# Kernel optimization log

Measured on AMD Instinct MI355X. Metric: run time of the kernel, lower is better.

The kernel has to match this reference:

```python
import jax, jax.numpy as jnp
import numpy as np

B, S, QS, KS, F, H = 4, 2048, 512, 1024, 1024, 16
DH = F // H  # head dim = 64


def setup_inputs() -> dict:
    key = jax.random.key(0)
    ks = jax.random.split(key, 7)
    s = 0.02
    return {
        "x": jax.random.normal(ks[0], (B, S, QS), dtype=jnp.float32),
        "y": jax.random.normal(ks[1], (B, S, QS), dtype=jnp.float32),
        "z": jax.random.normal(ks[2], (B, S, KS), dtype=jnp.float32),
        "Wq": jax.random.normal(ks[3], (2 * QS, F), dtype=jnp.float32) * s,
        "Wk": jax.random.normal(ks[4], (KS, F), dtype=jnp.float32) * s,
        "Wv": jax.random.normal(ks[5], (KS, F), dtype=jnp.float32) * s,
        "Wo": jax.random.normal(ks[6], (F, F), dtype=jnp.float32) * s,
    }


def _split_heads(t):
    # [B, S, F] -> [B, H, S, DH]
    return t.reshape(B, S, H, DH).transpose(0, 2, 1, 3)


def reference(x, y, z, Wq, Wk, Wv, Wo):
    q = _split_heads(jnp.concatenate([x, y], axis=-1) @ Wq)  # [B,H,S,DH]
    k = _split_heads(z @ Wk)
    v = _split_heads(z @ Wv)
    scale = 1.0 / jnp.sqrt(jnp.asarray(DH, dtype=q.dtype))
    scores = jnp.einsum("bhsd,bhtd->bhst", q, k) * scale  # [B,H,S,S]
    attn = jax.nn.softmax(scores, axis=-1)
    out = jnp.einsum("bhst,bhtd->bhsd", attn, v)  # [B,H,S,DH]
    out = out.transpose(0, 2, 1, 3).reshape(B, S, F)
    return out @ Wo
```

## Files before the change

kernel.cpp:

```cpp
#include <hip/hip_runtime.h>

typedef __attribute__((ext_vector_type(8))) short short8;
typedef __attribute__((ext_vector_type(4))) float f32x4;
typedef __attribute__((ext_vector_type(16))) float f32x16;
typedef __attribute__((ext_vector_type(4))) unsigned short us4;
typedef __attribute__((ext_vector_type(4))) unsigned int u32x4;

#define GLOAD16(gsrc, ldst)                                             \
  __builtin_amdgcn_global_load_lds(                                     \
      (const __attribute__((address_space(1))) unsigned int*)(gsrc),    \
      (__attribute__((address_space(3))) unsigned int*)(ldst), 16, 0, 0)

#define VMEM_DRAIN_BARRIER()                              \
  do {                                                    \
    asm volatile("s_waitcnt vmcnt(0)" ::: "memory");      \
    __builtin_amdgcn_sched_barrier(0);                    \
    __syncthreads();                                      \
  } while (0)

#if __has_builtin(__builtin_amdgcn_exp2f)
#define EXP2F(x) __builtin_amdgcn_exp2f(x)
#else
#define EXP2F(x) exp2f(x)
#endif

static __device__ __forceinline__ unsigned short f2bf(float f) {
  unsigned int u = __float_as_uint(f);
  u += 0x7fffu + ((u >> 16) & 1u);
  return (unsigned short)(u >> 16);
}

static __device__ __forceinline__ unsigned cvtpk(float lo, float hi) {
  unsigned r;
  asm("v_cvt_pk_bf16_f32 %0, %1, %2" : "=v"(r) : "v"(lo), "v"(hi));
  return r;
}

__global__ __launch_bounds__(256) void prep(const float* __restrict__ x,
                                            const float* __restrict__ y,
                                            const float* __restrict__ z,
                                            const float* __restrict__ Wq,
                                            const float* __restrict__ Wk,
                                            const float* __restrict__ Wv,
                                            const float* __restrict__ Wo,
                                            unsigned short* __restrict__ XY,
                                            unsigned short* __restrict__ Z,
                                            unsigned short* __restrict__ WqT,
                                            unsigned short* __restrict__ WkT,
                                            unsigned short* __restrict__ WvT,
                                            unsigned short* __restrict__ WoT) {
  __shared__ __align__(16) unsigned short LT[64 * 72];
  const int bid = blockIdx.x, t = threadIdx.x;

  if (bid < 2048) {
    const int NX = (8192 * 512) / 4;
    const int NZ = (8192 * 1024) / 4;
    const int total = 2 * NX + NZ;
    for (int idx = bid * 256 + t; idx < total; idx += 2048 * 256) {
      const float* src;
      unsigned short* dst;
      if (idx < NX) {
        int p = idx * 4; int row = p >> 9, c = p & 511;
        src = x + p; dst = XY + (size_t)row * 1024 + c;
      } else if (idx < 2 * NX) {
        int p = (idx - NX) * 4; int row = p >> 9, c = p & 511;
        src = y + p; dst = XY + (size_t)row * 1024 + 512 + c;
      } else {
        int p = (idx - 2 * NX) * 4;
        src = z + p; dst = Z + p;
      }
      float4 v = *(const float4*)src;
      us4 o; o[0] = f2bf(v.x); o[1] = f2bf(v.y); o[2] = f2bf(v.z); o[3] = f2bf(v.w);
      *(us4*)dst = o;
    }
    return;
  }

  const int seg = (bid - 2048) >> 8;
  const int local = (bid - 2048) & 255;
  const float* W = (seg == 0) ? Wq : (seg == 1) ? Wk : (seg == 2) ? Wv : Wo;
  unsigned short* WT = (seg == 0) ? WqT : (seg == 1) ? WkT : (seg == 2) ? WvT : WoT;
  const int k0 = (local >> 4) * 64, n0 = (local & 15) * 64;
#pragma unroll
  for (int j = 0; j < 4; ++j) {
    int r = j * 16 + (t >> 4);
    int c = (t & 15) * 4;
    float4 w = *(const float4*)(W + (size_t)(k0 + r) * 1024 + n0 + c);
    LT[(c + 0) * 72 + r] = f2bf(w.x);
    LT[(c + 1) * 72 + r] = f2bf(w.y);
    LT[(c + 2) * 72 + r] = f2bf(w.z);
    LT[(c + 3) * 72 + r] = f2bf(w.w);
  }
  __syncthreads();
#pragma unroll
  for (int j = 0; j < 2; ++j) {
    int n = j * 32 + (t >> 3), ch = t & 7;
    *(short8*)(WT + (size_t)(n0 + n) * 1024 + k0 + ch * 8) =
        *(const short8*)(LT + n * 72 + ch * 8);
  }
}

__global__ __launch_bounds__(256) void qkv_gemm(const unsigned short* __restrict__ XY,
                                                const unsigned short* __restrict__ Zb,
                                                const unsigned short* __restrict__ WqT,
                                                const unsigned short* __restrict__ WkT,
                                                const unsigned short* __restrict__ WvT,
                                                unsigned short* __restrict__ Qb,
                                                unsigned short* __restrict__ Kb,
                                                unsigned short* __restrict__ Vb) {
  __shared__ __align__(16) unsigned short As[2][128 * 32];
  __shared__ __align__(16) unsigned short Bs[2][128 * 32];
  const int tid = threadIdx.x;
  const int lane = tid & 63, wid = tid >> 6;
  const int lq = lane & 15, lg = lane >> 4;
  const int wr = wid >> 1, wc = wid & 1;
  const int seg = blockIdx.x >> 3;
  const int m0 = blockIdx.y * 128, n0 = (blockIdx.x & 7) * 128;

  const unsigned short* A;
  const unsigned short* Bt;
  unsigned short* C;
  float scale;
  if (seg == 0)      { A = XY; Bt = WqT; C = Qb; scale = 0.18033688011112042f; }
  else if (seg == 1) { A = Zb; Bt = WkT; C = Kb; scale = 1.0f; }
  else               { A = Zb; Bt = WvT; C = Vb; scale = 1.0f; }

  const int sr = tid >> 2, sc = tid & 3;

#define GSTAGE(bf, kk)                                                       \
  do {                                                                       \
    _Pragma("unroll")                                                        \
    for (int i = 0; i < 2; ++i) {                                            \
      int r = i * 64 + sr;                                                   \
      int c = sc ^ ((r >> 1) & 3);                                           \
      GLOAD16(A + (size_t)(m0 + r) * 1024 + (kk) + c * 8,                    \
              (char*)As[bf] + wid * 1024 + i * 4096);                        \
      GLOAD16(Bt + (size_t)(n0 + r) * 1024 + (kk) + c * 8,                   \
              (char*)Bs[bf] + wid * 1024 + i * 4096);                        \
    }                                                                        \
  } while (0)

  f32x4 acc[4][4] = {};
  GSTAGE(0, 0);
  VMEM_DRAIN_BARRIER();
  int buf = 0;

  for (int k0 = 0; k0 < 1024; k0 += 32) {
    if (k0 + 32 < 1024) GSTAGE(buf ^ 1, k0 + 32);
    short8 af[4], bfr[4];
#pragma unroll
    for (int mf = 0; mf < 4; ++mf) {
      int r = wr * 64 + mf * 16 + lq;
      int c = lg ^ ((r >> 1) & 3);
      af[mf] = *(const short8*)(As[buf] + r * 32 + c * 8);
    }
#pragma unroll
    for (int nf = 0; nf < 4; ++nf) {
      int r = wc * 64 + nf * 16 + lq;
      int c = lg ^ ((r >> 1) & 3);
      bfr[nf] = *(const short8*)(Bs[buf] + r * 32 + c * 8);
    }
#pragma unroll
    for (int mf = 0; mf < 4; ++mf)
#pragma unroll
      for (int nf = 0; nf < 4; ++nf)
        acc[mf][nf] = __builtin_amdgcn_mfma_f32_16x16x32_bf16(af[mf], bfr[nf],
                                                              acc[mf][nf], 0, 0, 0);
    VMEM_DRAIN_BARRIER();
    buf ^= 1;
  }
#undef GSTAGE

#pragma unroll
  for (int mf = 0; mf < 4; ++mf)
#pragma unroll
    for (int nf = 0; nf < 4; ++nf)
#pragma unroll
      for (int j = 0; j < 4; ++j) {
        int row = m0 + wr * 64 + mf * 16 + lg * 4 + j;
        int col = n0 + wc * 64 + nf * 16 + lq;
        C[(size_t)row * 1024 + col] = f2bf(acc[mf][nf][j] * scale);
      }
}

__global__ __launch_bounds__(256) void gemm_nt(const unsigned short* __restrict__ A,
                                               const unsigned short* __restrict__ Bt,
                                               float* __restrict__ Cout) {
  __shared__ __align__(16) unsigned short As[2][128 * 32];
  __shared__ __align__(16) unsigned short Bs[2][128 * 32];
  const int tid = threadIdx.x;
  const int lane = tid & 63, wid = tid >> 6;
  const int lq = lane & 15, lg = lane >> 4;
  const int wr = wid >> 1, wc = wid & 1;
  const int m0 = blockIdx.y * 128, n0 = blockIdx.x * 128;
  const int sr = tid >> 2, sc = tid & 3;

#define GSTAGE(bf, kk)                                                       \
  do {                                                                       \
    _Pragma("unroll")                                                        \
    for (int i = 0; i < 2; ++i) {                                            \
      int r = i * 64 + sr;                                                   \
      int c = sc ^ ((r >> 1) & 3);                                           \
      GLOAD16(A + (size_t)(m0 + r) * 1024 + (kk) + c * 8,                    \
              (char*)As[bf] + wid * 1024 + i * 4096);                        \
      GLOAD16(Bt + (size_t)(n0 + r) * 1024 + (kk) + c * 8,                   \
              (char*)Bs[bf] + wid * 1024 + i * 4096);                        \
    }                                                                        \
  } while (0)

  f32x4 acc[4][4] = {};
  GSTAGE(0, 0);
  VMEM_DRAIN_BARRIER();
  int buf = 0;

  for (int k0 = 0; k0 < 1024; k0 += 32) {
    if (k0 + 32 < 1024) GSTAGE(buf ^ 1, k0 + 32);
    short8 af[4], bfr[4];
#pragma unroll
    for (int mf = 0; mf < 4; ++mf) {
      int r = wr * 64 + mf * 16 + lq;
      int c = lg ^ ((r >> 1) & 3);
      af[mf] = *(const short8*)(As[buf] + r * 32 + c * 8);
    }
#pragma unroll
    for (int nf = 0; nf < 4; ++nf) {
      int r = wc * 64 + nf * 16 + lq;
      int c = lg ^ ((r >> 1) & 3);
      bfr[nf] = *(const short8*)(Bs[buf] + r * 32 + c * 8);
    }
#pragma unroll
    for (int mf = 0; mf < 4; ++mf)
#pragma unroll
      for (int nf = 0; nf < 4; ++nf)
        acc[mf][nf] = __builtin_amdgcn_mfma_f32_16x16x32_bf16(af[mf], bfr[nf],
                                                              acc[mf][nf], 0, 0, 0);
    VMEM_DRAIN_BARRIER();
    buf ^= 1;
  }
#undef GSTAGE

#pragma unroll
  for (int mf = 0; mf < 4; ++mf)
#pragma unroll
    for (int nf = 0; nf < 4; ++nf)
#pragma unroll
      for (int j = 0; j < 4; ++j) {
        int row = m0 + wr * 64 + mf * 16 + lg * 4 + j;
        int col = n0 + wc * 64 + nf * 16 + lq;
        Cout[(size_t)row * 1024 + col] = acc[mf][nf][j];
      }
}

__global__ __launch_bounds__(256) void vtrans(const unsigned short* __restrict__ V,
                                              unsigned short* __restrict__ Vt) {
  __shared__ __align__(16) unsigned short LT[64 * 72];
  const int bh = blockIdx.y, b = bh >> 4, h = bh & 15;
  const int s0 = blockIdx.x * 64;
  const int t = threadIdx.x;
#pragma unroll
  for (int i = 0; i < 2; ++i) {
    int r = i * 32 + (t >> 3);
    int c = t & 7;
    short8 v = *(const short8*)(V + (size_t)(b * 2048 + s0 + r) * 1024 + h * 64 + c * 8);
#pragma unroll
    for (int e = 0; e < 8; ++e)
      LT[(c * 8 + e) * 72 + r] = (unsigned short)v[e];
  }
  __syncthreads();
#pragma unroll
  for (int i = 0; i < 2; ++i) {
    int d = i * 32 + (t >> 3);
    int c = t & 7;
    *(short8*)(Vt + ((size_t)bh * 64 + d) * 2048 + s0 + c * 8) =
        *(const short8*)(LT + d * 72 + c * 8);
  }
}

__global__ __launch_bounds__(256, 4) void attn7(const unsigned short* __restrict__ Q,
                                                const unsigned short* __restrict__ K,
                                                const unsigned short* __restrict__ Vt,
                                                unsigned short* __restrict__ AO) {
  __shared__ __align__(16) unsigned short Ks[2][64 * 64];
  __shared__ __align__(16) unsigned short Vs[2][64 * 64];

  const int lin = blockIdx.x + (blockIdx.y << 4);
  const int xcd = lin & 7, rest = lin >> 3;
  const int bh = xcd * 8 + (rest >> 4);
  const int q0 = (rest & 15) * 128;
  const int b = bh >> 4, h = bh & 15;

  const int tid = threadIdx.x, lane = tid & 63, w = tid >> 6;
  const int l31 = lane & 31, hi = lane >> 5;
  const int swz = l31 & 7;

  short8 qf[4];
#pragma unroll
  for (int dblk = 0; dblk < 4; ++dblk)
    qf[dblk] = *(const short8*)(Q + (size_t)(b * 2048 + q0 + w * 32 + l31) * 1024 +
                                h * 64 + dblk * 16 + hi * 8);

  short8 ones;
#pragma unroll
  for (int e = 0; e < 8; ++e) ones[e] = (short)0x3F80;

#define STAGE(bf, t)                                                               \
  do {                                                                             \
    _Pragma("unroll")                                                              \
    for (int i = 0; i < 2; ++i) {                                                  \
      int ch = i * 256 + tid;                                                      \
      int r = ch >> 3, c = ch & 7, g = c ^ (r & 7);                                \
      GLOAD16(K + (size_t)(b * 2048 + (t) * 64 + r) * 1024 + h * 64 + g * 8,       \
              (char*)Ks[bf] + i * 4096 + w * 1024);                                \
    }                                                                              \
    _Pragma("unroll")                                                              \
    for (int i = 0; i < 2; ++i) {                                                  \
      int ch = i * 256 + tid;                                                      \
      int r = ch >> 3, c = ch & 7, g = c ^ (r & 7);                                \
      GLOAD16(Vt + ((size_t)bh * 64 + r) * 2048 + (t) * 64 + g * 8,                \
              (char*)Vs[bf] + i * 4096 + w * 1024);                                \
    }                                                                              \
  } while (0)

  STAGE(0, 0);
  VMEM_DRAIN_BARRIER();

  f32x16 od[2] = {};
  f32x16 sums = {};
  int buf = 0;

  for (int t = 0; t < 32; ++t) {
    if (t < 31) STAGE(buf ^ 1, t + 1);

    f32x16 st[2];
    __builtin_amdgcn_s_setprio(1);
#pragma unroll
    for (int kh = 0; kh < 2; ++kh) {
      f32x16 a = {};
#pragma unroll
      for (int dblk = 0; dblk < 4; ++dblk) {
        short8 kf = *(const short8*)(Ks[buf] + (kh * 32 + l31) * 64 +
                                     (((dblk * 2 + hi) ^ swz) * 8));
        a = __builtin_amdgcn_mfma_f32_32x32x16_bf16(kf, qf[dblk], a, 0, 0, 0);
      }
      st[kh] = a;
    }
    __builtin_amdgcn_s_setprio(0);

#pragma unroll
    for (int kh = 0; kh < 2; ++kh)
#pragma unroll
      for (int r = 0; r < 16; ++r) st[kh][r] = EXP2F(st[kh][r]);

    __builtin_amdgcn_s_setprio(1);
#pragma unroll
    for (int ks = 0; ks < 4; ++ks) {
      const int tt = ks >> 1, cm = (ks & 1) * 2;
      unsigned a_lo = cvtpk(st[tt][cm * 4 + 0], st[tt][cm * 4 + 1]);
      unsigned a_hi = cvtpk(st[tt][cm * 4 + 2], st[tt][cm * 4 + 3]);
      unsigned b_lo = cvtpk(st[tt][cm * 4 + 4], st[tt][cm * 4 + 5]);
      unsigned b_hi = cvtpk(st[tt][cm * 4 + 6], st[tt][cm * 4 + 7]);
      auto Xlo = __builtin_amdgcn_permlane32_swap(a_lo, b_lo, false, false);
      auto Xhi = __builtin_amdgcn_permlane32_swap(a_hi, b_hi, false, false);
      u32x4 up;
      up[0] = Xlo[0];
      up[1] = Xhi[0];
      up[2] = Xlo[1];
      up[3] = Xhi[1];
      short8 pa = __builtin_bit_cast(short8, up);
      sums = __builtin_amdgcn_mfma_f32_32x32x16_bf16(ones, pa, sums, 0, 0, 0);
#pragma unroll
      for (int td = 0; td < 2; ++td) {
        short8 vf = *(const short8*)(Vs[buf] + (td * 32 + l31) * 64 +
                                     (((ks * 2 + hi) ^ swz) * 8));
        od[td] = __builtin_amdgcn_mfma_f32_32x32x16_bf16(vf, pa, od[td], 0, 0, 0);
      }
    }
    __builtin_amdgcn_s_setprio(0);

    VMEM_DRAIN_BARRIER();
    buf ^= 1;
  }

  float inv = 1.0f / sums[0];
  const size_t orow = (size_t)(b * 2048 + q0 + w * 32 + l31);
#pragma unroll
  for (int td = 0; td < 2; ++td)
#pragma unroll
    for (int rh = 0; rh < 4; ++rh) {
      us4 o4;
#pragma unroll
      for (int rl = 0; rl < 4; ++rl) o4[rl] = f2bf(od[td][rh * 4 + rl] * inv);
      *(us4*)(AO + orow * 1024 + h * 64 + td * 32 + rh * 8 + hi * 4) = o4;
    }
#undef STAGE
}

extern "C" void kernel_launch(void* const* d_in, const int* in_sizes, int n_in,
                              void* d_out, int out_size, void* d_ws, size_t ws_size,
                              hipStream_t stream) {
  const float* x = (const float*)d_in[0];
  const float* y = (const float*)d_in[1];
  const float* z = (const float*)d_in[2];
  const float* Wq = (const float*)d_in[3];
  const float* Wk = (const float*)d_in[4];
  const float* Wv = (const float*)d_in[5];
  const float* Wo = (const float*)d_in[6];

  char* ws = (char*)d_ws;
  unsigned short* XY  = (unsigned short*)(ws + 0);
  unsigned short* Zb  = (unsigned short*)(ws + 16777216);
  unsigned short* WqT = (unsigned short*)(ws + 33554432);
  unsigned short* WkT = (unsigned short*)(ws + 35651584);
  unsigned short* WvT = (unsigned short*)(ws + 37748736);
  unsigned short* WoT = (unsigned short*)(ws + 39845888);
  unsigned short* Qb  = (unsigned short*)(ws + 41943040);
  unsigned short* Kb  = (unsigned short*)(ws + 58720256);
  unsigned short* Vb  = (unsigned short*)(ws + 75497472);
  unsigned short* Vtg = (unsigned short*)(ws + 92274688);
  unsigned short* AO  = (unsigned short*)(ws + 109051904);

  prep<<<3072, 256, 0, stream>>>(x, y, z, Wq, Wk, Wv, Wo,
                                 XY, Zb, WqT, WkT, WvT, WoT);

  qkv_gemm<<<dim3(24, 64), 256, 0, stream>>>(XY, Zb, WqT, WkT, WvT, Qb, Kb, Vb);

  vtrans<<<dim3(32, 64), 256, 0, stream>>>(Vb, Vtg);
  attn7<<<dim3(16, 64), 256, 0, stream>>>(Qb, Kb, Vtg, AO);

  gemm_nt<<<dim3(8, 64), 256, 0, stream>>>(AO, WoT, (float*)d_out);
}
```

Measured before the change: 223.6 us.

## Triple-buffer LDS pipelines with partial vmcnt waits and remap block grids

The QKV GEMM, output GEMM and attention kernels move from double-buffered LDS staging with a full vmcnt drain to three-stage buffering. Each iteration prefetches two tiles ahead and waits only on the older loads, keeping global loads in flight across the MFMA work. Block indices are remapped so that blocks sharing operands land on the same XCD. The attention kernel now uses 512-thread blocks covering 256 query rows, which halves K/V staging per query. The costs are more LDS per block, two barriers per iteration, and possibly lower occupancy.

```diff
diff --git a/kernel.cpp b/kernel.cpp
--- a/kernel.cpp
+++ b/kernel.cpp
@@ -11,12 +11,9 @@
       (const __attribute__((address_space(1))) unsigned int*)(gsrc),    \
       (__attribute__((address_space(3))) unsigned int*)(ldst), 16, 0, 0)
 
-#define VMEM_DRAIN_BARRIER()                              \
-  do {                                                    \
-    asm volatile("s_waitcnt vmcnt(0)" ::: "memory");      \
-    __builtin_amdgcn_sched_barrier(0);                    \
-    __syncthreads();                                      \
-  } while (0)
+#define SB() __builtin_amdgcn_sched_barrier(0)
+#define BAR() __builtin_amdgcn_s_barrier()
+#define WAITV(N) asm volatile("s_waitcnt vmcnt(" #N ")" ::: "memory")
 
 #if __has_builtin(__builtin_amdgcn_exp2f)
 #define EXP2F(x) __builtin_amdgcn_exp2f(x)
@@ -108,14 +105,18 @@
                                                 unsigned short* __restrict__ Qb,
                                                 unsigned short* __restrict__ Kb,
                                                 unsigned short* __restrict__ Vb) {
-  __shared__ __align__(16) unsigned short As[2][128 * 32];
-  __shared__ __align__(16) unsigned short Bs[2][128 * 32];
+  __shared__ __align__(16) unsigned short As[3][128 * 32];
+  __shared__ __align__(16) unsigned short Bs[3][128 * 32];
   const int tid = threadIdx.x;
   const int lane = tid & 63, wid = tid >> 6;
   const int lq = lane & 15, lg = lane >> 4;
   const int wr = wid >> 1, wc = wid & 1;
-  const int seg = blockIdx.x >> 3;
-  const int m0 = blockIdx.y * 128, n0 = (blockIdx.x & 7) * 128;
+
+  const int lin = blockIdx.x + blockIdx.y * 24;
+  const int xcd = lin & 7, rr = lin >> 3;
+  const int gp = xcd * 3 + (rr >> 6);
+  const int seg = gp >> 3;
+  const int m0 = (rr & 63) * 128, n0 = (gp & 7) * 128;
 
   const unsigned short* A;
   const unsigned short* Bt;
@@ -142,23 +143,33 @@
 
   f32x4 acc[4][4] = {};
   GSTAGE(0, 0);
-  VMEM_DRAIN_BARRIER();
-  int buf = 0;
-
-  for (int k0 = 0; k0 < 1024; k0 += 32) {
-    if (k0 + 32 < 1024) GSTAGE(buf ^ 1, k0 + 32);
+  GSTAGE(1, 32);
+  int cur = 0, stg = 2;
+
+  for (int t = 0; t < 32; ++t) {
+    SB();
+    BAR();
+    SB();
+    if (t < 30) GSTAGE(stg, (t + 2) * 32);
+    if (t < 30)       WAITV(8);
+    else if (t == 30) WAITV(4);
+    else              WAITV(0);
+    SB();
+    BAR();
+    SB();
+
     short8 af[4], bfr[4];
 #pragma unroll
     for (int mf = 0; mf < 4; ++mf) {
       int r = wr * 64 + mf * 16 + lq;
       int c = lg ^ ((r >> 1) & 3);
-      af[mf] = *(const short8*)(As[buf] + r * 32 + c * 8);
+      af[mf] = *(const short8*)(As[cur] + r * 32 + c * 8);
     }
 #pragma unroll
     for (int nf = 0; nf < 4; ++nf) {
       int r = wc * 64 + nf * 16 + lq;
       int c = lg ^ ((r >> 1) & 3);
-      bfr[nf] = *(const short8*)(Bs[buf] + r * 32 + c * 8);
+      bfr[nf] = *(const short8*)(Bs[cur] + r * 32 + c * 8);
     }
 #pragma unroll
     for (int mf = 0; mf < 4; ++mf)
@@ -166,8 +177,8 @@
       for (int nf = 0; nf < 4; ++nf)
         acc[mf][nf] = __builtin_amdgcn_mfma_f32_16x16x32_bf16(af[mf], bfr[nf],
                                                               acc[mf][nf], 0, 0, 0);
-    VMEM_DRAIN_BARRIER();
-    buf ^= 1;
+    cur = (cur == 2) ? 0 : cur + 1;
+    stg = (stg == 2) ? 0 : stg + 1;
   }
 #undef GSTAGE
 
@@ -186,13 +197,15 @@
 __global__ __launch_bounds__(256) void gemm_nt(const unsigned short* __restrict__ A,
                                                const unsigned short* __restrict__ Bt,
                                                float* __restrict__ Cout) {
-  __shared__ __align__(16) unsigned short As[2][128 * 32];
-  __shared__ __align__(16) unsigned short Bs[2][128 * 32];
+  __shared__ __align__(16) unsigned short As[3][128 * 32];
+  __shared__ __align__(16) unsigned short Bs[3][128 * 32];
   const int tid = threadIdx.x;
   const int lane = tid & 63, wid = tid >> 6;
   const int lq = lane & 15, lg = lane >> 4;
   const int wr = wid >> 1, wc = wid & 1;
-  const int m0 = blockIdx.y * 128, n0 = blockIdx.x * 128;
+  const int lin = blockIdx.x + blockIdx.y * 8;
+  const int n0 = (lin & 7) * 128;
+  const int m0 = (lin >> 3) * 128;
   const int sr = tid >> 2, sc = tid & 3;
 
 #define GSTAGE(bf, kk)                                                       \
@@ -210,23 +223,33 @@
 
   f32x4 acc[4][4] = {};
   GSTAGE(0, 0);
-  VMEM_DRAIN_BARRIER();
-  int buf = 0;
-
-  for (int k0 = 0; k0 < 1024; k0 += 32) {
-    if (k0 + 32 < 1024) GSTAGE(buf ^ 1, k0 + 32);
+  GSTAGE(1, 32);
+  int cur = 0, stg = 2;
+
+  for (int t = 0; t < 32; ++t) {
+    SB();
+    BAR();
+    SB();
+    if (t < 30) GSTAGE(stg, (t + 2) * 32);
+    if (t < 30)       WAITV(8);
+    else if (t == 30) WAITV(4);
+    else              WAITV(0);
+    SB();
+    BAR();
+    SB();
+
     short8 af[4], bfr[4];
 #pragma unroll
     for (int mf = 0; mf < 4; ++mf) {
       int r = wr * 64 + mf * 16 + lq;
       int c = lg ^ ((r >> 1) & 3);
-      af[mf] = *(const short8*)(As[buf] + r * 32 + c * 8);
+      af[mf] = *(const short8*)(As[cur] + r * 32 + c * 8);
     }
 #pragma unroll
     for (int nf = 0; nf < 4; ++nf) {
       int r = wc * 64 + nf * 16 + lq;
       int c = lg ^ ((r >> 1) & 3);
-      bfr[nf] = *(const short8*)(Bs[buf] + r * 32 + c * 8);
+      bfr[nf] = *(const short8*)(Bs[cur] + r * 32 + c * 8);
     }
 #pragma unroll
     for (int mf = 0; mf < 4; ++mf)
@@ -234,8 +257,8 @@
       for (int nf = 0; nf < 4; ++nf)
         acc[mf][nf] = __builtin_amdgcn_mfma_f32_16x16x32_bf16(af[mf], bfr[nf],
                                                               acc[mf][nf], 0, 0, 0);
-    VMEM_DRAIN_BARRIER();
-    buf ^= 1;
+    cur = (cur == 2) ? 0 : cur + 1;
+    stg = (stg == 2) ? 0 : stg + 1;
   }
 #undef GSTAGE
 
@@ -276,17 +299,17 @@
   }
 }
 
-__global__ __launch_bounds__(256, 4) void attn7(const unsigned short* __restrict__ Q,
+__global__ __launch_bounds__(512, 2) void attn9(const unsigned short* __restrict__ Q,
                                                 const unsigned short* __restrict__ K,
                                                 const unsigned short* __restrict__ Vt,
                                                 unsigned short* __restrict__ AO) {
-  __shared__ __align__(16) unsigned short Ks[2][64 * 64];
-  __shared__ __align__(16) unsigned short Vs[2][64 * 64];
-
-  const int lin = blockIdx.x + (blockIdx.y << 4);
+  __shared__ __align__(16) unsigned short Ks[3][64 * 64];
+  __shared__ __align__(16) unsigned short Vs[3][64 * 64];
+
+  const int lin = blockIdx.x + (blockIdx.y << 3);
   const int xcd = lin & 7, rest = lin >> 3;
-  const int bh = xcd * 8 + (rest >> 4);
-  const int q0 = (rest & 15) * 128;
+  const int bh = xcd * 8 + (rest >> 3);
+  const int q0 = (rest & 7) * 256;
   const int b = bh >> 4, h = bh & 15;
 
   const int tid = threadIdx.x, lane = tid & 63, w = tid >> 6;
@@ -305,31 +328,33 @@
 
 #define STAGE(bf, t)                                                               \
   do {                                                                             \
-    _Pragma("unroll")                                                              \
-    for (int i = 0; i < 2; ++i) {                                                  \
-      int ch = i * 256 + tid;                                                      \
-      int r = ch >> 3, c = ch & 7, g = c ^ (r & 7);                                \
+    {                                                                              \
+      int r = tid >> 3, c = tid & 7, g = c ^ (r & 7);                              \
       GLOAD16(K + (size_t)(b * 2048 + (t) * 64 + r) * 1024 + h * 64 + g * 8,       \
-              (char*)Ks[bf] + i * 4096 + w * 1024);                                \
-    }                                                                              \
-    _Pragma("unroll")                                                              \
-    for (int i = 0; i < 2; ++i) {                                                  \
-      int ch = i * 256 + tid;                                                      \
-      int r = ch >> 3, c = ch & 7, g = c ^ (r & 7);                                \
+              (char*)Ks[bf] + w * 1024);                                           \
       GLOAD16(Vt + ((size_t)bh * 64 + r) * 2048 + (t) * 64 + g * 8,                \
-              (char*)Vs[bf] + i * 4096 + w * 1024);                                \
+              (char*)Vs[bf] + w * 1024);                                           \
     }                                                                              \
   } while (0)
 
   STAGE(0, 0);
-  VMEM_DRAIN_BARRIER();
+  STAGE(1, 1);
+  int cur = 0, stg = 2;
 
   f32x16 od[2] = {};
   f32x16 sums = {};
-  int buf = 0;
 
   for (int t = 0; t < 32; ++t) {
-    if (t < 31) STAGE(buf ^ 1, t + 1);
+    SB();
+    BAR();
+    SB();
+    if (t < 30) STAGE(stg, t + 2);
+    if (t < 30)       WAITV(4);
+    else if (t == 30) WAITV(2);
+    else              WAITV(0);
+    SB();
+    BAR();
+    SB();
 
     f32x16 st[2];
     __builtin_amdgcn_s_setprio(1);
@@ -338,7 +363,7 @@
       f32x16 a = {};
 #pragma unroll
       for (int dblk = 0; dblk < 4; ++dblk) {
-        short8 kf = *(const short8*)(Ks[buf] + (kh * 32 + l31) * 64 +
+        short8 kf = *(const short8*)(Ks[cur] + (kh * 32 + l31) * 64 +
                                      (((dblk * 2 + hi) ^ swz) * 8));
         a = __builtin_amdgcn_mfma_f32_32x32x16_bf16(kf, qf[dblk], a, 0, 0, 0);
       }
@@ -370,15 +395,15 @@
       sums = __builtin_amdgcn_mfma_f32_32x32x16_bf16(ones, pa, sums, 0, 0, 0);
 #pragma unroll
       for (int td = 0; td < 2; ++td) {
-        short8 vf = *(const short8*)(Vs[buf] + (td * 32 + l31) * 64 +
+        short8 vf = *(const short8*)(Vs[cur] + (td * 32 + l31) * 64 +
                                      (((ks * 2 + hi) ^ swz) * 8));
         od[td] = __builtin_amdgcn_mfma_f32_32x32x16_bf16(vf, pa, od[td], 0, 0, 0);
       }
     }
     __builtin_amdgcn_s_setprio(0);
 
-    VMEM_DRAIN_BARRIER();
-    buf ^= 1;
+    cur = (cur == 2) ? 0 : cur + 1;
+    stg = (stg == 2) ? 0 : stg + 1;
   }
 
   float inv = 1.0f / sums[0];
@@ -425,7 +450,7 @@
   qkv_gemm<<<dim3(24, 64), 256, 0, stream>>>(XY, Zb, WqT, WkT, WvT, Qb, Kb, Vb);
 
   vtrans<<<dim3(32, 64), 256, 0, stream>>>(Vb, Vtg);
-  attn7<<<dim3(16, 64), 256, 0, stream>>>(Qb, Kb, Vtg, AO);
+  attn9<<<dim3(8, 64), 512, 0, stream>>>(Qb, Kb, Vtg, AO);
 
   gemm_nt<<<dim3(8, 64), 256, 0, stream>>>(AO, WoT, (float*)d_out);
 }
```

New measurement: 207.6 us. 1.08x faster.
